# Optimization experiments

Hardware: AMD Instinct MI355X
Metric: run time of the kernel (lower is better)

## Reference

```python
import jax, jax.numpy as jnp
import numpy as np

N_NODES = 50000
N_EDGES = 800000
NODE_IN = 256
EDGE_IN = 64
HEADS = 4
OUT = 64
NEG_SLOPE = 0.2  # dgl GATConv default


def setup_inputs() -> dict:
    key = jax.random.key(0)
    ks = jax.random.split(key, 10)
    node_feats = jax.random.normal(ks[0], (N_NODES, NODE_IN), dtype=jnp.float32)
    edge_feats = jax.random.normal(ks[1], (N_EDGES, EDGE_IN), dtype=jnp.float32)
    src = jax.random.randint(ks[2], (N_EDGES,), 0, N_NODES, dtype=jnp.int32)
    dst = jax.random.randint(ks[3], (N_EDGES,), 0, N_NODES, dtype=jnp.int32)
    # learned params (Xavier-ish scaling)
    W = jax.random.normal(ks[4], (NODE_IN, HEADS * OUT), dtype=jnp.float32) / np.sqrt(NODE_IN)
    We = jax.random.normal(ks[5], (EDGE_IN, HEADS * OUT), dtype=jnp.float32) / np.sqrt(EDGE_IN)
    attn_l = jax.random.normal(ks[6], (HEADS, OUT), dtype=jnp.float32) / np.sqrt(OUT)
    attn_r = jax.random.normal(ks[7], (HEADS, OUT), dtype=jnp.float32) / np.sqrt(OUT)
    attn_e = jax.random.normal(ks[8], (HEADS, OUT), dtype=jnp.float32) / np.sqrt(OUT)
    return {"node_feats": node_feats, "edge_feats": edge_feats, "W": W, "We": We,
            "attn_l": attn_l, "attn_r": attn_r, "attn_e": attn_e, "src": src, "dst": dst}


def reference(node_feats, edge_feats, W, We, attn_l, attn_r, attn_e, src, dst):
    # GAT with edge features (dropout disabled for deterministic reference).
    N = node_feats.shape[0]
    H, D = attn_l.shape
    h = (node_feats @ W).reshape(N, H, D)              # [N,H,D] projected nodes
    fe = (edge_feats @ We).reshape(-1, H, D)           # [E,H,D] projected edges
    el = jnp.sum(h * attn_l, axis=-1)                  # [N,H]
    er = jnp.sum(h * attn_r, axis=-1)                  # [N,H]
    ee = jnp.sum(fe * attn_e, axis=-1)                 # [E,H]
    e = jax.nn.leaky_relu(el[src] + er[dst] + ee, NEG_SLOPE)  # [E,H]
    # numerically stable segment softmax over incoming edges of each dst node
    emax = jax.ops.segment_max(e, dst, num_segments=N)         # [N,H]
    emax = jnp.where(jnp.isfinite(emax), emax, 0.0)            # empty segments -> 0
    ex = jnp.exp(e - emax[dst])                                # [E,H]
    denom = jax.ops.segment_sum(ex, dst, num_segments=N)       # [N,H]
    alpha = ex / (denom[dst] + 1e-9)                           # [E,H]
    out = jax.ops.segment_sum(alpha[..., None] * h[src], dst, num_segments=N)  # [N,H,D]
    return out
```

## Files before the change

kernel.cpp:

```cpp
#include <hip/hip_runtime.h>
#include <hip/hip_bf16.h>
#include <math.h>

#define N_NODES 50000
#define N_EDGES 800000
#define HEADS 4
#define HD 256
#define NEG_SLOPE 0.2f

typedef __attribute__((ext_vector_type(8))) short bf16x8;
typedef __attribute__((ext_vector_type(4))) float f32x4;

struct __align__(32) EPack {
    float ex[4];
    int   s;
    int   pad[3];
};

__device__ unsigned short g_Hb[N_NODES * HD];
__device__ float    g_el[N_NODES * HEADS];
__device__ float    g_er[N_NODES * HEADS];
__device__ EPack    g_ep[N_EDGES];
__device__ int      g_deg[N_NODES];
__device__ int      g_rowptr[N_NODES + 1];
__device__ int      g_cursor[N_NODES];
__device__ int      g_bsum[256];
__device__ float    g_Wea[64 * HEADS];
__device__ unsigned short g_Wbt[256 * 256];
__device__ unsigned short g_Wlrb[16 * 256];

__device__ __forceinline__ unsigned short f2bf(float f) {
    unsigned u = __float_as_uint(f);
    u += 0x7fffu + ((u >> 16) & 1u);
    return (unsigned short)(u >> 16);
}
__device__ __forceinline__ float bf_lo(unsigned u) {
    return __uint_as_float(u << 16);
}
__device__ __forceinline__ float bf_hi(unsigned u) {
    return __uint_as_float(u & 0xFFFF0000u);
}

__global__ void k_zero() {
    int g = blockIdx.x * 256 + threadIdx.x;
    if (g < N_NODES) g_deg[g] = 0;
}

__global__ void k_prep(const float* __restrict__ W, const float* __restrict__ We,
                       const float* __restrict__ al, const float* __restrict__ ar,
                       const float* __restrict__ ae, const int* __restrict__ dst) {
    int t = blockIdx.x * 256 + threadIdx.x;
    if (t < 256) {
        int k = t >> 2, h = t & 3;
        float s = 0.f;
        for (int d = 0; d < 64; ++d) s += We[k * 256 + h * 64 + d] * ae[h * 64 + d];
        g_Wea[t] = s;
    }
    if (t < 4096) {
        int c = t >> 8, k = t & 255;
        float s = 0.f;
        if (c < 4) {
            for (int d = 0; d < 64; ++d) s += W[k * 256 + c * 64 + d] * al[c * 64 + d];
        } else if (c < 8) {
            int h = c - 4;
            for (int d = 0; d < 64; ++d) s += W[k * 256 + h * 64 + d] * ar[h * 64 + d];
        }
        g_Wlrb[c * 256 + k] = f2bf(s);
    }
    for (int i = t; i < 65536; i += 50176) {
        int n = i >> 8, k = i & 255;
        g_Wbt[n * 256 + k] = f2bf(W[k * 256 + n]);
    }
    for (int e = t; e < N_EDGES; e += 50176)
        atomicAdd(&g_deg[dst[e]], 1);
}

#define BM 128
#define BK 64
__global__ __launch_bounds__(256) void k_gemm_mfma(const float* __restrict__ X) {
    __shared__ unsigned short As[BM][BK + 8];
    const int tid = threadIdx.x;
    const int wave = tid >> 6, lane = tid & 63;
    const int l15 = lane & 15, lg = lane >> 4;
    const int row0 = blockIdx.x * BM;
    const int slab = blockIdx.y;

    f32x4 acc[8][2];
    f32x4 accE[8];
    #pragma unroll
    for (int i = 0; i < 8; ++i) {
        accE[i] = (f32x4){0.f, 0.f, 0.f, 0.f};
        #pragma unroll
        for (int j = 0; j < 2; ++j) acc[i][j] = (f32x4){0.f, 0.f, 0.f, 0.f};
    }

    for (int k0 = 0; k0 < 256; k0 += BK) {
        #pragma unroll
        for (int q = 0; q < 8; ++q) {
            int f = q * 256 + tid;
            int r = f >> 4;
            int kq = (f & 15) << 2;
            int grow = row0 + r;
            float4 v = make_float4(0.f, 0.f, 0.f, 0.f);
            if (grow < N_NODES) v = *(const float4*)(X + grow * 256 + k0 + kq);
            ushort4 b;
            b.x = f2bf(v.x); b.y = f2bf(v.y); b.z = f2bf(v.z); b.w = f2bf(v.w);
            *(ushort4*)&As[r][kq] = b;
        }
        bf16x8 bfr[2][2], bfrE[2];
        #pragma unroll
        for (int kk = 0; kk < 2; ++kk) {
            #pragma unroll
            for (int nf = 0; nf < 2; ++nf) {
                int n = slab * 128 + wave * 32 + nf * 16 + l15;
                bfr[kk][nf] = *(const bf16x8*)(g_Wbt + n * 256 + k0 + kk * 32 + lg * 8);
            }
            bfrE[kk] = *(const bf16x8*)(g_Wlrb + l15 * 256 + k0 + kk * 32 + lg * 8);
        }
        __syncthreads();
        #pragma unroll
        for (int kk = 0; kk < 2; ++kk) {
            #pragma unroll
            for (int mf = 0; mf < 8; ++mf) {
                bf16x8 afr = *(const bf16x8*)&As[mf * 16 + l15][kk * 32 + lg * 8];
                #pragma unroll
                for (int nf = 0; nf < 2; ++nf)
                    acc[mf][nf] = __builtin_amdgcn_mfma_f32_16x16x32_bf16(
                        afr, bfr[kk][nf], acc[mf][nf], 0, 0, 0);
                if (slab == 0)
                    accE[mf] = __builtin_amdgcn_mfma_f32_16x16x32_bf16(
                        afr, bfrE[kk], accE[mf], 0, 0, 0);
            }
        }
        __syncthreads();
    }
    #pragma unroll
    for (int mf = 0; mf < 8; ++mf) {
        #pragma unroll
        for (int r = 0; r < 4; ++r) {
            int grow = row0 + mf * 16 + lg * 4 + r;
            if (grow < N_NODES) {
                #pragma unroll
                for (int nf = 0; nf < 2; ++nf) {
                    int col = slab * 128 + wave * 32 + nf * 16 + l15;
                    g_Hb[grow * 256 + col] = f2bf(acc[mf][nf][r]);
                }
                if (slab == 0 && wave == 0) {
                    if (l15 < 4) g_el[grow * 4 + l15] = accE[mf][r];
                    else if (l15 < 8) g_er[grow * 4 + (l15 - 4)] = accE[mf][r];
                }
            }
        }
    }
}

__global__ void k_scan1() {
    __shared__ int s[256];
    int tid = threadIdx.x;
    int g = blockIdx.x * 256 + tid;
    int v = (g < N_NODES) ? g_deg[g] : 0;
    s[tid] = v; __syncthreads();
    for (int o = 1; o < 256; o <<= 1) {
        int t = (tid >= o) ? s[tid - o] : 0;
        __syncthreads();
        s[tid] += t;
        __syncthreads();
    }
    if (g < N_NODES) g_rowptr[g] = s[tid] - v;
    if (tid == 255) g_bsum[blockIdx.x] = s[255];
}

__global__ void k_scan2(int nb) {
    __shared__ int s[256];
    int tid = threadIdx.x;
    int v = (tid < nb) ? g_bsum[tid] : 0;
    s[tid] = v; __syncthreads();
    for (int o = 1; o < 256; o <<= 1) {
        int t = (tid >= o) ? s[tid - o] : 0;
        __syncthreads();
        s[tid] += t;
        __syncthreads();
    }
    if (tid < nb) g_bsum[tid] = s[tid] - v;
}

__global__ void k_scan3() {
    int g = blockIdx.x * 256 + threadIdx.x;
    if (g < N_NODES) {
        int r = g_rowptr[g] + g_bsum[blockIdx.x];
        g_rowptr[g] = r;
        g_cursor[g] = r;
    }
    if (g == 0) g_rowptr[N_NODES] = N_EDGES;
}

__global__ __launch_bounds__(256) void k_edge(const float* __restrict__ EF,
                                              const int* __restrict__ src,
                                              const int* __restrict__ dst) {
    __shared__ float sEF[32][258];
    __shared__ float4 sW[64];
    const int tid = threadIdx.x;
    if (tid < 64) sW[tid] = *(const float4*)(g_Wea + tid * 4);
    const int e0 = blockIdx.x * 256;

    float p0 = 0.f, p1 = 0.f, p2 = 0.f, p3 = 0.f;
    #pragma unroll
    for (int kc = 0; kc < 2; ++kc) {
        __syncthreads();
        #pragma unroll
        for (int q = 0; q < 8; ++q) {
            int f = q * 256 + tid;
            int e = f >> 3;
            int c = (f & 7) << 2;
            float4 v = *(const float4*)(EF + (size_t)(e0 + e) * 64 + kc * 32 + c);
            sEF[c + 0][e] = v.x; sEF[c + 1][e] = v.y;
            sEF[c + 2][e] = v.z; sEF[c + 3][e] = v.w;
        }
        __syncthreads();
        #pragma unroll
        for (int k = 0; k < 32; ++k) {
            float x = sEF[k][tid];
            float4 w = sW[kc * 32 + k];
            p0 += x * w.x; p1 += x * w.y; p2 += x * w.z; p3 += x * w.w;
        }
    }
    const int eid = e0 + tid;
    const int s = src[eid], d = dst[eid];
    float4 l4 = *(const float4*)(g_el + s * 4);
    float4 r4 = *(const float4*)(g_er + d * 4);
    float e0v = p0 + l4.x + r4.x;
    float e1v = p1 + l4.y + r4.y;
    float e2v = p2 + l4.z + r4.z;
    float e3v = p3 + l4.w + r4.w;
    e0v = e0v > 0.f ? e0v : NEG_SLOPE * e0v;
    e1v = e1v > 0.f ? e1v : NEG_SLOPE * e1v;
    e2v = e2v > 0.f ? e2v : NEG_SLOPE * e2v;
    e3v = e3v > 0.f ? e3v : NEG_SLOPE * e3v;
    int p = atomicAdd(&g_cursor[d], 1);
    *(float4*)g_ep[p].ex =
        make_float4(__expf(e0v), __expf(e1v), __expf(e2v), __expf(e3v));
    g_ep[p].s = s;
}

__global__ __launch_bounds__(256) void k_agg(float* __restrict__ out) {
    int node = (blockIdx.x * 256 + threadIdx.x) >> 6;
    int lane = threadIdx.x & 63;
    if (node >= N_NODES) return;
    int start = g_rowptr[node], end = g_rowptr[node + 1];
    int myh = lane >> 4, sub = lane & 15;
    const int hoff = myh * 64 + sub * 4;

    float den = 0.f;
    float a0 = 0.f, a1 = 0.f, a2 = 0.f, a3 = 0.f;
    #pragma unroll 8
    for (int i = start; i < end; ++i) {
        float ex = g_ep[i].ex[myh];
        int s = g_ep[i].s;
        uint2 hv = *(const uint2*)(g_Hb + s * 256 + hoff);
        den += ex;
        a0 += ex * bf_lo(hv.x); a1 += ex * bf_hi(hv.x);
        a2 += ex * bf_lo(hv.y); a3 += ex * bf_hi(hv.y);
    }
    float rden = 1.0f / (den + 1e-9f);
    *(float4*)(out + node * 256 + lane * 4) =
        make_float4(a0 * rden, a1 * rden, a2 * rden, a3 * rden);
}

extern "C" void kernel_launch(void* const* d_in, const int* in_sizes, int n_in,
                              void* d_out, int out_size, void* d_ws, size_t ws_size,
                              hipStream_t stream) {
    const float* X  = (const float*)d_in[0];
    const float* EF = (const float*)d_in[1];
    const float* W  = (const float*)d_in[2];
    const float* We = (const float*)d_in[3];
    const float* al = (const float*)d_in[4];
    const float* ar = (const float*)d_in[5];
    const float* ae = (const float*)d_in[6];
    const int* src  = (const int*)d_in[7];
    const int* dst  = (const int*)d_in[8];
    float* out = (float*)d_out;

    const int nb_scan = (N_NODES + 255) / 256;

    k_zero<<<nb_scan, 256, 0, stream>>>();
    k_prep<<<nb_scan, 256, 0, stream>>>(W, We, al, ar, ae, dst);
    k_gemm_mfma<<<dim3((N_NODES + BM - 1) / BM, 2), 256, 0, stream>>>(X);
    k_scan1<<<nb_scan, 256, 0, stream>>>();
    k_scan2<<<1, 256, 0, stream>>>(nb_scan);
    k_scan3<<<nb_scan, 256, 0, stream>>>();
    k_edge<<<N_EDGES / 256, 256, 0, stream>>>(EF, src, dst);
    k_agg<<<(N_NODES + 3) / 4, 256, 0, stream>>>(out);
}
```

Measured before the change: 247.1 us.

## Split agg edges across wave halves, merge scan kernels, use nontemporal loads

Each wave in the aggregation kernel now splits a node's incoming edges between its two 32-lane halves. Each lane gathers 16-byte bf16 chunks, and the halves combine their partial sums with cross-lane shuffles. The aim is more outstanding memory requests and wider gathers. The second and third scan kernels are merged into one, with every block redundantly rescanning the block sums, which removes a launch. Edge-feature and edge-pack reads and the output store now use nontemporal hints to cut cache pollution.

```diff
diff --git a/kernel.cpp b/kernel.cpp
--- a/kernel.cpp
+++ b/kernel.cpp
@@ -10,6 +10,7 @@
 
 typedef __attribute__((ext_vector_type(8))) short bf16x8;
 typedef __attribute__((ext_vector_type(4))) float f32x4;
+typedef __attribute__((ext_vector_type(4))) unsigned int u32x4;
 
 struct __align__(32) EPack {
     float ex[4];
@@ -170,24 +171,21 @@
     if (tid == 255) g_bsum[blockIdx.x] = s[255];
 }
 
-__global__ void k_scan2(int nb) {
-    __shared__ int s[256];
+__global__ void k_scan3(int nb) {
+    __shared__ int sb[256];
     int tid = threadIdx.x;
     int v = (tid < nb) ? g_bsum[tid] : 0;
-    s[tid] = v; __syncthreads();
+    sb[tid] = v; __syncthreads();
     for (int o = 1; o < 256; o <<= 1) {
-        int t = (tid >= o) ? s[tid - o] : 0;
-        __syncthreads();
-        s[tid] += t;
-        __syncthreads();
-    }
-    if (tid < nb) g_bsum[tid] = s[tid] - v;
-}
-
-__global__ void k_scan3() {
-    int g = blockIdx.x * 256 + threadIdx.x;
+        int t = (tid >= o) ? sb[tid - o] : 0;
+        __syncthreads();
+        sb[tid] += t;
+        __syncthreads();
+    }
+    int boff = sb[blockIdx.x] - g_bsum[blockIdx.x];
+    int g = blockIdx.x * 256 + tid;
     if (g < N_NODES) {
-        int r = g_rowptr[g] + g_bsum[blockIdx.x];
+        int r = g_rowptr[g] + boff;
         g_rowptr[g] = r;
         g_cursor[g] = r;
     }
@@ -212,7 +210,8 @@
             int f = q * 256 + tid;
             int e = f >> 3;
             int c = (f & 7) << 2;
-            float4 v = *(const float4*)(EF + (size_t)(e0 + e) * 64 + kc * 32 + c);
+            f32x4 v = __builtin_nontemporal_load(
+                (const f32x4*)(EF + (size_t)(e0 + e) * 64 + kc * 32 + c));
             sEF[c + 0][e] = v.x; sEF[c + 1][e] = v.y;
             sEF[c + 2][e] = v.z; sEF[c + 3][e] = v.w;
         }
@@ -247,23 +246,31 @@
     int lane = threadIdx.x & 63;
     if (node >= N_NODES) return;
     int start = g_rowptr[node], end = g_rowptr[node + 1];
-    int myh = lane >> 4, sub = lane & 15;
-    const int hoff = myh * 64 + sub * 4;
+    const int half = lane >> 5;
+    const int hl = lane & 31;
+    const int myh = hl >> 3, sub = lane & 7;
+    const int hoff = myh * 64 + sub * 8;
 
     float den = 0.f;
-    float a0 = 0.f, a1 = 0.f, a2 = 0.f, a3 = 0.f;
-    #pragma unroll 8
-    for (int i = start; i < end; ++i) {
-        float ex = g_ep[i].ex[myh];
-        int s = g_ep[i].s;
-        uint2 hv = *(const uint2*)(g_Hb + s * 256 + hoff);
+    float a[8] = {};
+    #pragma unroll 4
+    for (int i = start + half; i < end; i += 2) {
+        float ex = __builtin_nontemporal_load(&g_ep[i].ex[myh]);
+        int s    = __builtin_nontemporal_load(&g_ep[i].s);
+        u32x4 hv = *(const u32x4*)(g_Hb + s * 256 + hoff);
         den += ex;
-        a0 += ex * bf_lo(hv.x); a1 += ex * bf_hi(hv.x);
-        a2 += ex * bf_lo(hv.y); a3 += ex * bf_hi(hv.y);
-    }
+        a[0] += ex * bf_lo(hv.x); a[1] += ex * bf_hi(hv.x);
+        a[2] += ex * bf_lo(hv.y); a[3] += ex * bf_hi(hv.y);
+        a[4] += ex * bf_lo(hv.z); a[5] += ex * bf_hi(hv.z);
+        a[6] += ex * bf_lo(hv.w); a[7] += ex * bf_hi(hv.w);
+    }
+    den += __shfl_xor(den, 32);
+    #pragma unroll
+    for (int k = 0; k < 8; ++k) a[k] += __shfl_xor(a[k], 32);
     float rden = 1.0f / (den + 1e-9f);
-    *(float4*)(out + node * 256 + lane * 4) =
-        make_float4(a0 * rden, a1 * rden, a2 * rden, a3 * rden);
+    f32x4 o = half ? (f32x4){a[4] * rden, a[5] * rden, a[6] * rden, a[7] * rden}
+                   : (f32x4){a[0] * rden, a[1] * rden, a[2] * rden, a[3] * rden};
+    __builtin_nontemporal_store(o, (f32x4*)(out + node * 256 + hoff + half * 4));
 }
 
 extern "C" void kernel_launch(void* const* d_in, const int* in_sizes, int n_in,
@@ -286,8 +293,7 @@
     k_prep<<<nb_scan, 256, 0, stream>>>(W, We, al, ar, ae, dst);
     k_gemm_mfma<<<dim3((N_NODES + BM - 1) / BM, 2), 256, 0, stream>>>(X);
     k_scan1<<<nb_scan, 256, 0, stream>>>();
-    k_scan2<<<1, 256, 0, stream>>>(nb_scan);
-    k_scan3<<<nb_scan, 256, 0, stream>>>();
+    k_scan3<<<nb_scan, 256, 0, stream>>>(nb_scan);
     k_edge<<<N_EDGES / 256, 256, 0, stream>>>(EF, src, dst);
     k_agg<<<(N_NODES + 3) / 4, 256, 0, stream>>>(out);
 }
```

Result: no change. 243.7 us (-1.4%).
